# Kernel optimization log

Hardware: AMD Instinct MI355X
Metric: run time of the kernel (lower is better)

The kernel has to match this reference:

```python
import jax, jax.numpy as jnp
import numpy as np

K = 3
VOCAB = 32000
EMBED = 1024
SEQ_LEN = 256
BATCH = 8


def setup_inputs() -> dict:
    key = jax.random.key(0)
    k1, k2, k3 = jax.random.split(key, 3)
    tokens_seq = jax.random.randint(k1, (SEQ_LEN, BATCH), 0, VOCAB, dtype=jnp.int64 if jax.config.jax_enable_x64 else jnp.int32)
    W1 = jax.random.normal(k2, (K * VOCAB, EMBED), dtype=jnp.float32) * 0.02
    b1 = jnp.zeros((EMBED,), dtype=jnp.float32)
    W2 = jax.random.normal(k3, (EMBED, VOCAB), dtype=jnp.float32) * 0.02
    b2 = jnp.zeros((VOCAB,), dtype=jnp.float32)
    return {"tokens_seq": tokens_seq, "W1": W1, "b1": b1, "W2": W2, "b2": b2}


def reference(tokens_seq, W1, b1, W2, b2):
    # tokens_seq: (S, B). Context for position t is [pad...] + tokens[t-K:t] (zeros pad).
    S, B = tokens_seq.shape
    padded = jnp.concatenate([jnp.zeros((K, B), dtype=tokens_seq.dtype), tokens_seq], axis=0)  # (S+K, B)
    # one_hot(context).flatten() @ W1 == sum_j W1_rows[j, context_j]
    W1r = W1.reshape(K, VOCAB, EMBED)  # slot-major flatten order matches F.one_hot(...).flatten()
    h = b1
    for j in range(K):  # K is a small compile-time constant
        ctx_j = padded[j:j + S]           # (S, B): j-th slot of each context window
        h = h + W1r[j][ctx_j]             # gather rows: (S, B, E)
    h = jax.nn.relu(h)
    logits = jnp.einsum('sbe,ev->sbv', h, W2) + b2  # (S, B, V)
    return logits
```

## Files before the change

kernel.cpp:

```cpp
#include <hip/hip_runtime.h>
#include <hip/hip_bf16.h>

#define VOCAB 32000
#define EMBED 1024
#define SEQ 256
#define BATCH 8
#define ROWS (SEQ * BATCH)

#define BM 256
#define BN 256
#define BK 64
#define NT (EMBED / BK)

typedef short short8 __attribute__((ext_vector_type(8)));
typedef float f32x4 __attribute__((ext_vector_type(4)));

__device__ __forceinline__ unsigned short f2bf(float f) {
    __hip_bfloat16 h = __float2bfloat16(f);
    return *reinterpret_cast<unsigned short*>(&h);
}

#define GLOAD_LDS16(gsrc, ldst)                                                        \
    __builtin_amdgcn_global_load_lds((const __attribute__((address_space(1))) void*)(gsrc), \
                                     (__attribute__((address_space(3))) void*)(ldst), 16, 0, 0)

__global__ __launch_bounds__(256) void prep_k(const int* __restrict__ toks,
                                              const float* __restrict__ W1,
                                              const float* __restrict__ b1,
                                              const float* __restrict__ W2,
                                              unsigned short* __restrict__ h,
                                              unsigned short* __restrict__ W2t) {
    __shared__ float tile[64][65];
    int bid = blockIdx.x;
    int t = threadIdx.x;
    if (bid < 8000) {
        int n0 = (bid % 500) * 64;
        int k0 = (bid / 500) * 64;
        int tx = t & 15, ty = t >> 4;
#pragma unroll
        for (int p = 0; p < 4; ++p) {
            int k = ty + p * 16;
            float4 v = *(const float4*)(W2 + (size_t)(k0 + k) * VOCAB + n0 + tx * 4);
            tile[k][tx * 4 + 0] = v.x; tile[k][tx * 4 + 1] = v.y;
            tile[k][tx * 4 + 2] = v.z; tile[k][tx * 4 + 3] = v.w;
        }
        __syncthreads();
        int kx = t & 15, ny = t >> 4;
#pragma unroll
        for (int p = 0; p < 4; ++p) {
            int n = ny + p * 16;
            int k = kx * 4;
            union { unsigned short u[4]; uint2 v; } o;
            o.u[0] = f2bf(tile[k + 0][n]); o.u[1] = f2bf(tile[k + 1][n]);
            o.u[2] = f2bf(tile[k + 2][n]); o.u[3] = f2bf(tile[k + 3][n]);
            *(uint2*)(W2t + (size_t)(n0 + n) * EMBED + k0 + k) = o.v;
        }
    } else {
        int r = bid - 8000;
        int s = r >> 3, b = r & 7;
        int t0 = (s >= 3) ? toks[(s - 3) * BATCH + b] : 0;
        int t1 = (s >= 2) ? toks[(s - 2) * BATCH + b] : 0;
        int t2 = (s >= 1) ? toks[(s - 1) * BATCH + b] : 0;
        int e = t * 4;
        float4 vb = *(const float4*)(b1 + e);
        float4 v0 = *(const float4*)(W1 + ((size_t)0 * VOCAB + t0) * EMBED + e);
        float4 v1 = *(const float4*)(W1 + ((size_t)1 * VOCAB + t1) * EMBED + e);
        float4 v2 = *(const float4*)(W1 + ((size_t)2 * VOCAB + t2) * EMBED + e);
        float x0 = fmaxf(vb.x + v0.x + v1.x + v2.x, 0.0f);
        float x1 = fmaxf(vb.y + v0.y + v1.y + v2.y, 0.0f);
        float x2 = fmaxf(vb.z + v0.z + v1.z + v2.z, 0.0f);
        float x3 = fmaxf(vb.w + v0.w + v1.w + v2.w, 0.0f);
        union { unsigned short u[4]; uint2 v; } o;
        o.u[0] = f2bf(x0); o.u[1] = f2bf(x1); o.u[2] = f2bf(x2); o.u[3] = f2bf(x3);
        *(uint2*)(h + (size_t)r * EMBED + e) = o.v;
    }
}

__global__ __launch_bounds__(512, 2) void gemm8_k(const unsigned short* __restrict__ A,
                                                  const unsigned short* __restrict__ B,
                                                  const float* __restrict__ b2,
                                                  float* __restrict__ out) {
    extern __shared__ char lds[];
    char* Al = lds;
    char* Bl = lds + 65536;

    int wg = blockIdx.x;
    int xcd = wg & 7, idx = wg >> 3;
    int wgid = (xcd < 4 ? xcd * 63 : 4 * 63 + (xcd - 4) * 62) + idx;
    int mg = wgid & 3;
    int n0 = (wgid >> 2) * BN;
    int m0 = mg * 512;

    int tid = threadIdx.x;
    int w = tid >> 6, lane = tid & 63;
    int wm = w >> 2, wn = w & 3;
    int ksw = ((lane & 7) ^ ((lane >> 3) & 7)) * 8;

    f32x4 acc[8][4] = {};
    short8 af[2][2], bfr[4][2];

    auto stage = [&](const unsigned short* __restrict__ g, int grow0, char* ldsbase, int t) {
#pragma unroll
        for (int j = 0; j < 2; ++j) {
            int c = j * 8 + w;
            int row = c * 8 + (lane >> 3);
            const unsigned short* src = g + (size_t)(grow0 + row) * EMBED + t * BK + ksw;
            GLOAD_LDS16(src, ldsbase + c * 1024);
        }
    };
    auto stA = [&](int buf, int hh, int t, int mbase) { stage(A, mbase + hh * 128, Al + buf * 32768 + hh * 16384, t); };
    auto stB = [&](int buf, int hh, int t) { stage(B, n0 + hh * 128, Bl + buf * 32768 + hh * 16384, t); };

    auto ldA = [&](int buf, int qq) {
#pragma unroll
        for (int i = 0; i < 2; ++i)
#pragma unroll
            for (int kk = 0; kk < 2; ++kk) {
                int row = wm * 128 + (qq * 2 + i) * 16 + (lane & 15);
                int cb = ((lane >> 4) * 16 + kk * 64) ^ ((lane & 7) << 4);
                af[i][kk] = *(const short8*)(Al + buf * 32768 + row * 128 + cb);
            }
    };
    auto ldB = [&](int buf) {
#pragma unroll
        for (int n = 0; n < 4; ++n)
#pragma unroll
            for (int kk = 0; kk < 2; ++kk) {
                int row = wn * 64 + n * 16 + (lane & 15);
                int cb = ((lane >> 4) * 16 + kk * 64) ^ ((lane & 7) << 4);
                bfr[n][kk] = *(const short8*)(Bl + buf * 32768 + row * 128 + cb);
            }
    };

#define MFMA_Q(q)                                                                             \
    __builtin_amdgcn_s_setprio(1);                                                            \
    _Pragma("unroll") for (int i = 0; i < 2; ++i)                                             \
        _Pragma("unroll") for (int n = 0; n < 4; ++n)                                         \
            _Pragma("unroll") for (int kk = 0; kk < 2; ++kk)                                  \
                acc[(q)*2 + i][n] = __builtin_amdgcn_mfma_f32_16x16x32_bf16(                  \
                    af[i][kk], bfr[n][kk], acc[(q)*2 + i][n], 0, 0, 0);                       \
    __builtin_amdgcn_s_setprio(0);

#define PH(ldbuf, q, DO_LDB, STAGE_STMT, WAITV)                                               \
    ldA(ldbuf, q);                                                                            \
    if (DO_LDB) ldB(ldbuf);                                                                   \
    STAGE_STMT;                                                                               \
    if (DO_LDB) asm volatile("s_waitcnt lgkmcnt(8)");                                         \
    if (WAITV) asm volatile("s_waitcnt vmcnt(4)");                                            \
    __builtin_amdgcn_s_barrier();                                                             \
    asm volatile("s_waitcnt lgkmcnt(0)");                                                     \
    MFMA_Q(q);                                                                                \
    __builtin_amdgcn_s_barrier();

    auto kloop = [&](int mcur) {
        for (int it = 0; it < NT / 2; ++it) {
            int t1 = (it * 2 + 1) & (NT - 1);
            int t2 = (it * 2 + 2) & (NT - 1);
            int t3 = (it * 2 + 3) & (NT - 1);
            PH(0, 0, true,  stA(1, 0, t1, mcur), false)
            PH(0, 1, false, stA(1, 1, t1, mcur), false)
            PH(0, 2, false, stB(0, 0, t2),       false)
            PH(0, 3, false, stB(0, 1, t2),       true)
            PH(1, 0, true,  stA(0, 0, t2, mcur), false)
            PH(1, 1, false, stA(0, 1, t2, mcur), false)
            PH(1, 2, false, stB(1, 0, t3),       false)
            PH(1, 3, false, stB(1, 1, t3),       true)
        }
    };

    int colq = lane & 15;
    int rowq = (lane >> 4) * 4;
    auto epi = [&](int mbase) {
#pragma unroll
        for (int nf = 0; nf < 4; ++nf) {
            int col = n0 + wn * 64 + nf * 16 + colq;
            float bias = b2[col];
#pragma unroll
            for (int mf = 0; mf < 8; ++mf) {
                int row0 = mbase + wm * 128 + mf * 16 + rowq;
#pragma unroll
                for (int q = 0; q < 4; ++q)
                    out[(size_t)(row0 + q) * VOCAB + col] = acc[mf][nf][q] + bias;
            }
        }
    };

    stA(0, 0, 0, m0); stA(0, 1, 0, m0); stB(0, 0, 0); stB(0, 1, 0);
    stB(1, 0, 1); stB(1, 1, 1);
    asm volatile("s_waitcnt vmcnt(4)");
    __builtin_amdgcn_s_barrier();

    kloop(m0);

    int m1 = m0 + 256;
    stA(0, 0, 0, m1); stA(0, 1, 0, m1);
    epi(m0);
    asm volatile("s_waitcnt vmcnt(63)" ::: "memory");
    __builtin_amdgcn_s_barrier();

#pragma unroll
    for (int mf = 0; mf < 8; ++mf)
#pragma unroll
        for (int nf = 0; nf < 4; ++nf)
            acc[mf][nf] = f32x4{0.f, 0.f, 0.f, 0.f};

    kloop(m1);
    epi(m1);
#undef PH
#undef MFMA_Q
}

__global__ __launch_bounds__(256) void gemm_k(const unsigned short* __restrict__ h,
                                              const unsigned short* __restrict__ W2t,
                                              const float* __restrict__ b2,
                                              float* __restrict__ out) {
    __shared__ unsigned short Alds[128 * 64];
    __shared__ unsigned short Blds[128 * 64];
    int m0 = blockIdx.x * 128;
    int n0 = blockIdx.y * 128;
    int tid = threadIdx.x;
    int wave = tid >> 6, lane = tid & 63;
    int wr = (wave >> 1) * 64;
    int wc = (wave & 1) * 64;
    int lrow = lane & 15;
    int khalf = (lane >> 4) * 8;
    f32x4 acc[4][4] = {};
    for (int kt = 0; kt < EMBED; kt += 64) {
#pragma unroll
        for (int i = 0; i < 4; ++i) {
            int base = (wave * 4 + i) * 1024;
            int lin = base + lane * 16;
            int row = lin >> 7;
            int colu = (lin & 127) >> 1;
            GLOAD_LDS16(h + (size_t)(m0 + row) * EMBED + kt + colu, (char*)Alds + base);
            GLOAD_LDS16(W2t + (size_t)(n0 + row) * EMBED + kt + colu, (char*)Blds + base);
        }
        __syncthreads();
#pragma unroll
        for (int kc = 0; kc < 2; ++kc) {
            short8 af[4], bf[4];
#pragma unroll
            for (int m = 0; m < 4; ++m)
                af[m] = *(const short8*)(Alds + (wr + m * 16 + lrow) * 64 + kc * 32 + khalf);
#pragma unroll
            for (int n = 0; n < 4; ++n)
                bf[n] = *(const short8*)(Blds + (wc + n * 16 + lrow) * 64 + kc * 32 + khalf);
#pragma unroll
            for (int m = 0; m < 4; ++m)
#pragma unroll
                for (int n = 0; n < 4; ++n)
                    acc[m][n] = __builtin_amdgcn_mfma_f32_16x16x32_bf16(af[m], bf[n], acc[m][n], 0, 0, 0);
        }
        __syncthreads();
    }
    int colq = lane & 15;
    int rowq = (lane >> 4) * 4;
#pragma unroll
    for (int m = 0; m < 4; ++m)
#pragma unroll
        for (int n = 0; n < 4; ++n) {
            int col = n0 + wc + n * 16 + colq;
            float bias = b2[col];
#pragma unroll
            for (int q = 0; q < 4; ++q)
                out[(size_t)(m0 + wr + m * 16 + rowq + q) * VOCAB + col] = acc[m][n][q] + bias;
        }
}

__global__ __launch_bounds__(256) void naive_k(const int* __restrict__ toks,
                                               const float* __restrict__ W1,
                                               const float* __restrict__ b1,
                                               const float* __restrict__ W2,
                                               const float* __restrict__ b2,
                                               float* __restrict__ out) {
    __shared__ float hs[8][1024];
    int r0 = blockIdx.x * 8;
    int e = threadIdx.x * 4;
    for (int rr = 0; rr < 8; ++rr) {
        int r = r0 + rr, s = r >> 3, b = r & 7;
        int t0 = (s >= 3) ? toks[(s - 3) * BATCH + b] : 0;
        int t1 = (s >= 2) ? toks[(s - 2) * BATCH + b] : 0;
        int t2 = (s >= 1) ? toks[(s - 1) * BATCH + b] : 0;
        float4 vb = *(const float4*)(b1 + e);
        float4 v0 = *(const float4*)(W1 + ((size_t)t0) * EMBED + e);
        float4 v1 = *(const float4*)(W1 + ((size_t)VOCAB + t1) * EMBED + e);
        float4 v2 = *(const float4*)(W1 + ((size_t)2 * VOCAB + t2) * EMBED + e);
        hs[rr][e + 0] = fmaxf(vb.x + v0.x + v1.x + v2.x, 0.0f);
        hs[rr][e + 1] = fmaxf(vb.y + v0.y + v1.y + v2.y, 0.0f);
        hs[rr][e + 2] = fmaxf(vb.z + v0.z + v1.z + v2.z, 0.0f);
        hs[rr][e + 3] = fmaxf(vb.w + v0.w + v1.w + v2.w, 0.0f);
    }
    __syncthreads();
    for (int v = threadIdx.x; v < VOCAB; v += 256) {
        float acc[8];
#pragma unroll
        for (int i = 0; i < 8; ++i) acc[i] = b2[v];
        for (int ee = 0; ee < EMBED; ++ee) {
            float wv = W2[(size_t)ee * VOCAB + v];
#pragma unroll
            for (int i = 0; i < 8; ++i) acc[i] += hs[i][ee] * wv;
        }
#pragma unroll
        for (int i = 0; i < 8; ++i) out[(size_t)(r0 + i) * VOCAB + v] = acc[i];
    }
}

extern "C" void kernel_launch(void* const* d_in, const int* in_sizes, int n_in,
                              void* d_out, int out_size, void* d_ws, size_t ws_size,
                              hipStream_t stream) {
    const int* toks = (const int*)d_in[0];
    const float* W1 = (const float*)d_in[1];
    const float* b1 = (const float*)d_in[2];
    const float* W2 = (const float*)d_in[3];
    const float* b2 = (const float*)d_in[4];
    float* out = (float*)d_out;

    const size_t h_bytes = (size_t)ROWS * EMBED * 2;
    const size_t w2t_bytes = (size_t)VOCAB * EMBED * 2;
    if (ws_size >= h_bytes + w2t_bytes) {
        unsigned short* h = (unsigned short*)d_ws;
        unsigned short* W2t = (unsigned short*)((char*)d_ws + h_bytes);
        prep_k<<<8000 + ROWS, 256, 0, stream>>>(toks, W1, b1, W2, h, W2t);
        hipError_t e = hipFuncSetAttribute(reinterpret_cast<const void*>(gemm8_k),
                                           hipFuncAttributeMaxDynamicSharedMemorySize, 131072);
        if (e == hipSuccess) {
            gemm8_k<<<(ROWS / 512) * (VOCAB / BN), 512, 131072, stream>>>(h, W2t, b2, out);
        } else {
            gemm_k<<<dim3(ROWS / 128, VOCAB / 128), 256, 0, stream>>>(h, W2t, b2, out);
        }
    } else {
        naive_k<<<ROWS / 8, 256, 0, stream>>>(toks, W1, b1, W2, b2, out);
    }
}
```

Before: 205.6 us.

## Stage GEMM epilogue through LDS for coalesced nontemporal 16-byte output stores

The epilogue now writes accumulator fragments plus bias into an LDS staging region, 32 rows at a time, with barriers between steps. Each wave then reads back full rows and writes them to global memory as contiguous 16-byte nontemporal stores, where before it issued scattered 4-byte stores. This targets write coalescing on the large fp32 logits output. The cost is 16 extra barriers per epilogue, LDS traffic, and a possible conflict with the A-tile prefetch already issued into LDS. The vmcnt wait threshold was also lowered to match the new count of outstanding stores.

New measurement: 178.3 us. -13.3%, faster.

```diff
diff --git a/kernel.cpp b/kernel.cpp
--- a/kernel.cpp
+++ b/kernel.cpp
@@ -169,18 +169,36 @@
     };
 
     int colq = lane & 15;
-    int rowq = (lane >> 4) * 4;
+    int rowq4 = (lane >> 4) * 4;
     auto epi = [&](int mbase) {
-#pragma unroll
-        for (int nf = 0; nf < 4; ++nf) {
-            int col = n0 + wn * 64 + nf * 16 + colq;
-            float bias = b2[col];
-#pragma unroll
-            for (int mf = 0; mf < 8; ++mf) {
-                int row0 = mbase + wm * 128 + mf * 16 + rowq;
-#pragma unroll
-                for (int q = 0; q < 4; ++q)
-                    out[(size_t)(row0 + q) * VOCAB + col] = acc[mf][nf][q] + bias;
+        char* T = Al + 32768;
+        float bias[4];
+#pragma unroll
+        for (int nf = 0; nf < 4; ++nf) bias[nf] = b2[n0 + wn * 64 + nf * 16 + colq];
+#pragma unroll
+        for (int p = 0; p < 8; ++p) {
+            __builtin_amdgcn_s_barrier();
+            if (wm == (p >> 2)) {
+#pragma unroll
+                for (int mi = 0; mi < 2; ++mi) {
+                    int mf = (p & 3) * 2 + mi;
+                    int rl = mi * 16 + rowq4;
+#pragma unroll
+                    for (int nf = 0; nf < 4; ++nf) {
+                        int c = wn * 64 + nf * 16 + colq;
+#pragma unroll
+                        for (int q = 0; q < 4; ++q)
+                            *(float*)(T + (rl + q) * 1024 + c * 4) = acc[mf][nf][q] + bias[nf];
+                    }
+                }
+            }
+            __builtin_amdgcn_s_barrier();
+#pragma unroll
+            for (int rr = 0; rr < 4; ++rr) {
+                int rl = w * 4 + rr;
+                f32x4 v = *(const f32x4*)(T + rl * 1024 + lane * 16);
+                int grow = mbase + p * 32 + rl;
+                __builtin_nontemporal_store(v, (f32x4*)(out + (size_t)grow * VOCAB + n0 + lane * 4));
             }
         }
     };
@@ -195,7 +213,7 @@
     int m1 = m0 + 256;
     stA(0, 0, 0, m1); stA(0, 1, 0, m1);
     epi(m0);
-    asm volatile("s_waitcnt vmcnt(63)" ::: "memory");
+    asm volatile("s_waitcnt vmcnt(32)" ::: "memory");
     __builtin_amdgcn_s_barrier();
 
 #pragma unroll
```
